# Kernel optimization log

Measured on AMD Instinct MI355X. Metric: run time of the kernel, lower is better.

## Reference

```python
import jax, jax.numpy as jnp
import numpy as np

ALPHA = 0.5  # distance-decay base (self.alpha)

def setup_inputs() -> dict:
    key = jax.random.key(0)
    N, E, D_IN, D_OUT = 50000, 800000, 128, 128
    k1, k2, k3, k4, k5 = jax.random.split(key, 5)
    h = jax.random.normal(k1, (N, D_IN), dtype=jnp.float32)
    # first N edges are self-loops so every node has in/out degree >= 1
    src = jnp.concatenate([jnp.arange(N), jax.random.randint(k2, (E - N,), 0, N)]).astype(jnp.int32)
    dst = jnp.concatenate([jnp.arange(N), jax.random.randint(k3, (E - N,), 0, N)]).astype(jnp.int32)
    distance = jax.random.randint(k4, (E,), 0, 6).astype(jnp.int32)
    limit = float(np.sqrt(6.0 / (D_IN + D_OUT)))  # xavier_uniform
    weight = jax.random.uniform(k5, (D_IN, D_OUT), jnp.float32, -limit, limit)
    bias = jnp.zeros((D_OUT,), jnp.float32)
    return {"h": h, "src": src, "dst": dst, "distance": distance, "weight": weight, "bias": bias}

def reference(h, src, dst, distance, weight, bias):
    N = h.shape[0]
    ones = jnp.ones(src.shape[0], jnp.float32)
    out_deg = jax.ops.segment_sum(ones, src, num_segments=N)  # [N]
    in_deg = jax.ops.segment_sum(ones, dst, num_segments=N)   # [N]
    # source-side symmetric norm
    feat = h * (out_deg ** -0.5)[:, None]                     # [N, D]
    # per-edge message: gathered src feature * alpha^distance
    w = jnp.power(jnp.float32(ALPHA), distance.astype(jnp.float32))  # [E]
    msg = feat[src] * w[:, None]                              # [E, D]
    # mean over mailbox == segment-sum / in-degree
    agg = jax.ops.segment_sum(msg, dst, num_segments=N) / in_deg[:, None]  # [N, D]
    rst = agg @ weight                                        # [N, D_OUT]
    rst = rst * (in_deg ** -0.5)[:, None] + bias
    return rst
```

## Files before the change

### kernel.cpp

```cpp
#include <hip/hip_runtime.h>


constexpr int D = 128;
constexpr int HC = 32;
constexpr int PNODES = 32;
constexpr int PCAP = 768;
constexpr int CHUNK = 8192;
constexpr int NCAST = 384;

typedef __attribute__((ext_vector_type(8))) short bf16x8;
typedef __attribute__((ext_vector_type(4))) float f32x4;
typedef __attribute__((ext_vector_type(2))) _Float16 f16x2;

__device__ __forceinline__ float bf16_to_f(unsigned int u16) {
    union { unsigned int u; float f; } c; c.u = u16 << 16; return c.f;
}
__device__ __forceinline__ unsigned int f_to_bf16(float f) {
    union { float f; unsigned int u; } c; c.f = f;
    unsigned int u = c.u;
    u += 0x7fffu + ((u >> 16) & 1u);
    return u >> 16;
}
__device__ __forceinline__ unsigned int pack_f16x2(float x, float y) {
    f16x2 p; p.x = (_Float16)x; p.y = (_Float16)y;
    union { f16x2 h; unsigned int u; } c; c.h = p; return c.u;
}

__global__ __launch_bounds__(256) void k_combo(const int* __restrict__ src,
        const int* __restrict__ dst, const int* __restrict__ dist,
        int* __restrict__ gcur, unsigned int* __restrict__ gbuf,
        unsigned int* __restrict__ gdeg,
        const float4* __restrict__ h4, uint4* __restrict__ hs4,
        const float* __restrict__ W, unsigned short* __restrict__ Wt,
        int E, int N, int NW, int hchunk, int P, int nbA) {
    extern __shared__ int dyn[];
    int tid = threadIdx.x;
    int bi = blockIdx.x;

    if (bi >= nbA + HC) {
        if (bi == nbA + HC) {
            for (int i = tid; i < D * D; i += 256) {
                int k = i >> 7, n = i & 127;
                Wt[n * D + k] = (unsigned short)f_to_bf16(W[i]);
            }
            return;
        }
        int cb = bi - (nbA + HC + 1);
        int G = N * (D / 8);
        for (int i = cb * 256 + tid; i < G; i += NCAST * 256) {
            float4 a = h4[2 * i];
            float4 b = h4[2 * i + 1];
            uint4 o;
            o.x = pack_f16x2(a.x, a.y);
            o.y = pack_f16x2(a.z, a.w);
            o.z = pack_f16x2(b.x, b.y);
            o.w = pack_f16x2(b.z, b.w);
            hs4[i] = o;
        }
        return;
    }

    if (bi >= nbA) {
        unsigned int* bins = (unsigned int*)dyn;
        for (int i = tid; i < NW; i += 256) bins[i] = 0;
        __syncthreads();
        int c = bi - nbA;
        int e0 = c * hchunk, e1 = min(e0 + hchunk, E);
        for (int i = e0 + tid * 4; i < e1; i += 1024) {
            if (i + 3 < e1) {
                int4 k4 = *(const int4*)&src[i];
                atomicAdd(&bins[k4.x >> 1], 1u << ((k4.x & 1) * 16));
                atomicAdd(&bins[k4.y >> 1], 1u << ((k4.y & 1) * 16));
                atomicAdd(&bins[k4.z >> 1], 1u << ((k4.z & 1) * 16));
                atomicAdd(&bins[k4.w >> 1], 1u << ((k4.w & 1) * 16));
            } else {
                for (int e = i; e < e1; e++)
                    atomicAdd(&bins[src[e] >> 1], 1u << ((src[e] & 1) * 16));
            }
        }
        __syncthreads();
        for (int i = tid; i < NW; i += 256) {
            unsigned int v = bins[i];
            if (v) atomicAdd(&gdeg[i], v);
        }
        return;
    }

    unsigned int* sorted = (unsigned int*)dyn;
    int* gidx  = dyn + CHUNK;
    int* hist  = dyn + 2 * CHUNK;
    int* start = hist + P;
    int* lofs  = start + P;
    int* base_g = lofs + P;
    __shared__ int wsum[4];

    int lane = tid & 63, w = tid >> 6;
    int e0 = bi * CHUNK;
    int e1 = min(e0 + CHUNK, E);
    int ce = e1 - e0;

    for (int b = tid; b < P; b += 256) hist[b] = 0;
    __syncthreads();

    for (int i = e0 + tid * 4; i < e1; i += 1024) {
        if (i + 3 < e1) {
            int4 d4 = *(const int4*)&dst[i];
            atomicAdd(&hist[d4.x >> 5], 1);
            atomicAdd(&hist[d4.y >> 5], 1);
            atomicAdd(&hist[d4.z >> 5], 1);
            atomicAdd(&hist[d4.w >> 5], 1);
        } else {
            for (int e = i; e < e1; e++) atomicAdd(&hist[dst[e] >> 5], 1);
        }
    }
    __syncthreads();

    int loc[7];
    int s = 0;
    #pragma unroll
    for (int j = 0; j < 7; j++) {
        int b = tid * 7 + j;
        int v = (b < P) ? hist[b] : 0;
        loc[j] = s;
        s += v;
    }
    int x = s;
    #pragma unroll
    for (int off = 1; off < 64; off <<= 1) {
        int t = __shfl_up(x, off, 64);
        if (lane >= off) x += t;
    }
    if (lane == 63) wsum[w] = x;
    __syncthreads();
    int tbase = x - s;
    #pragma unroll
    for (int k = 0; k < 4; k++) if (k < w) tbase += wsum[k];
    #pragma unroll
    for (int j = 0; j < 7; j++) {
        int b = tid * 7 + j;
        if (b < P) {
            int st = tbase + loc[j];
            start[b] = st;
            lofs[b] = st;
            int cnt = hist[b];
            if (cnt) base_g[b] = atomicAdd(&gcur[b], cnt);
        }
    }
    __syncthreads();

    for (int i = e0 + tid * 4; i < e1; i += 1024) {
        if (i + 3 < e1) {
            int4 s4 = *(const int4*)&src[i];
            int4 d4 = *(const int4*)&dst[i];
            int4 q4 = *(const int4*)&dist[i];
            #pragma unroll
            for (int j = 0; j < 4; j++) {
                int sv = (&s4.x)[j], dv = (&d4.x)[j], qv = (&q4.x)[j];
                int p = dv >> 5;
                unsigned int wd = (unsigned)sv | ((unsigned)(dv & 31) << 16)
                                | ((unsigned)qv << 21);
                int pos = atomicAdd(&lofs[p], 1);
                sorted[pos] = wd;
                int rank = base_g[p] + (pos - start[p]);
                gidx[pos] = (rank < PCAP) ? p * PCAP + rank : -1;
            }
        } else {
            for (int e = i; e < e1; e++) {
                int sv = src[e], dv = dst[e], qv = dist[e];
                int p = dv >> 5;
                unsigned int wd = (unsigned)sv | ((unsigned)(dv & 31) << 16)
                                | ((unsigned)qv << 21);
                int pos = atomicAdd(&lofs[p], 1);
                sorted[pos] = wd;
                int rank = base_g[p] + (pos - start[p]);
                gidx[pos] = (rank < PCAP) ? p * PCAP + rank : -1;
            }
        }
    }
    __syncthreads();

    for (int i = tid; i < ce; i += 256) {
        int g = gidx[i];
        if (g >= 0) gbuf[g] = sorted[i];
    }
}

__global__ __launch_bounds__(256, 6) void k_pagg(const uint4* __restrict__ hs4,
        const unsigned int* __restrict__ gbuf, const int* __restrict__ gcur,
        const unsigned short* __restrict__ gdeg16,
        const unsigned short* __restrict__ Wt, const float* __restrict__ bias,
        float* __restrict__ out, int N) {
    __shared__ unsigned int elist[PCAP];
    __shared__ unsigned int slist[PCAP];
    __shared__ float scoef[PCAP];
    __shared__ int h2[PNODES], st2[PNODES], lo2[PNODES];
    __shared__ unsigned short As[PNODES * 136];
    int p = blockIdx.x;
    int tid = threadIdx.x;
    int cnt = min(gcur[p], PCAP);
    const unsigned int* gp = gbuf + (size_t)p * PCAP;

    if (tid < PNODES) h2[tid] = 0;
    __syncthreads();
    for (int i = tid; i < cnt; i += 256) {
        unsigned int wd = gp[i];
        elist[i] = wd;
        atomicAdd(&h2[(wd >> 16) & 31], 1);
    }
    __syncthreads();
    if (tid < 64) {
        int v = (tid < PNODES) ? h2[tid] : 0;
        int x = v;
        #pragma unroll
        for (int off = 1; off < 32; off <<= 1) {
            int t = __shfl_up(x, off, 64);
            if ((tid & 63) >= off) x += t;
        }
        if (tid < PNODES) { st2[tid] = x - v; lo2[tid] = x - v; }
    }
    __syncthreads();
    for (int i = tid; i < cnt; i += 256) {
        unsigned int wd = elist[i];
        int pos = atomicAdd(&lo2[(wd >> 16) & 31], 1);
        slist[pos] = wd;
        unsigned int sv = wd & 0xffffu;
        float os = rsqrtf((float)gdeg16[sv]);
        scoef[pos] = __uint_as_float((127u - ((wd >> 21) & 7u)) << 23) * os;
    }
    __syncthreads();

    int wv = tid >> 6, l64 = tid & 63;
    int lane16 = l64 & 15, sub = l64 >> 4;
    #pragma unroll
    for (int k = 0; k < 8; k++) {
        int dl = wv * 8 + k;
        int node = p * PNODES + dl;
        int deg = h2[dl], b = st2[dl];
        float acc[8] = {0.f, 0.f, 0.f, 0.f, 0.f, 0.f, 0.f, 0.f};
        for (int eo = 0; eo < deg; eo += 32) {
            uint4 hv[8];
            float cc[8];
            #pragma unroll
            for (int j = 0; j < 8; j++) {
                if (eo + j * 4 < deg) {
                    int off = eo + j * 4 + sub;
                    bool valid = off < deg;
                    int ei = b + (valid ? off : 0);
                    unsigned int wd = slist[ei];
                    float c0 = scoef[ei];
                    cc[j] = valid ? c0 : 0.f;
                    hv[j] = hs4[((wd & 0xffffu) << 4) + (unsigned)lane16];
                }
            }
            #pragma unroll
            for (int j = 0; j < 8; j++) {
                if (eo + j * 4 < deg) {
                    float c = cc[j];
                    const f16x2* hp = (const f16x2*)&hv[j];
                    #pragma unroll
                    for (int q = 0; q < 4; q++) {
                        acc[2 * q]     = fmaf((float)hp[q].x, c, acc[2 * q]);
                        acc[2 * q + 1] = fmaf((float)hp[q].y, c, acc[2 * q + 1]);
                    }
                }
            }
        }
        #pragma unroll
        for (int j = 0; j < 8; j++) {
            acc[j] += __shfl_xor(acc[j], 16, 64);
            acc[j] += __shfl_xor(acc[j], 32, 64);
        }
        if (sub == 0) {
            uint4 o = make_uint4(0u, 0u, 0u, 0u);
            if (node < N) {
                float fd = (float)deg;
                float sc = rsqrtf(fd) / fd;
                o.x = f_to_bf16(acc[0] * sc) | (f_to_bf16(acc[1] * sc) << 16);
                o.y = f_to_bf16(acc[2] * sc) | (f_to_bf16(acc[3] * sc) << 16);
                o.z = f_to_bf16(acc[4] * sc) | (f_to_bf16(acc[5] * sc) << 16);
                o.w = f_to_bf16(acc[6] * sc) | (f_to_bf16(acc[7] * sc) << 16);
            }
            *(uint4*)&As[dl * 136 + lane16 * 8] = o;
        }
    }
    __syncthreads();

    int m = l64 & 15, quad = l64 >> 4;
    int mt = wv & 1, ntb = (wv >> 1) * 4;
    f32x4 acc2[4];
    #pragma unroll
    for (int t = 0; t < 4; t++) acc2[t] = (f32x4){0.f, 0.f, 0.f, 0.f};
    #pragma unroll
    for (int s = 0; s < 4; s++) {
        bf16x8 a = *(const bf16x8*)&As[(mt * 16 + m) * 136 + quad * 8 + s * 32];
        #pragma unroll
        for (int t = 0; t < 4; t++) {
            int n = (ntb + t) * 16 + m;
            bf16x8 b = *(const bf16x8*)&Wt[n * D + quad * 8 + s * 32];
            acc2[t] = __builtin_amdgcn_mfma_f32_16x16x32_bf16(a, b, acc2[t], 0, 0, 0);
        }
    }
    int orow0 = p * PNODES + mt * 16 + quad * 4;
    #pragma unroll
    for (int t = 0; t < 4; t++) {
        int n = (ntb + t) * 16 + m;
        float bz = bias[n];
        #pragma unroll
        for (int r = 0; r < 4; r++) {
            int grow = orow0 + r;
            if (grow < N) out[(size_t)grow * D + n] = acc2[t][r] + bz;
        }
    }
}

extern "C" void kernel_launch(void* const* d_in, const int* in_sizes, int n_in,
                              void* d_out, int out_size, void* d_ws, size_t ws_size,
                              hipStream_t stream) {
    const float* h    = (const float*)d_in[0];
    const int*   src  = (const int*)d_in[1];
    const int*   dst  = (const int*)d_in[2];
    const int*   dist = (const int*)d_in[3];
    const float* W    = (const float*)d_in[4];
    const float* bias = (const float*)d_in[5];
    float* out = (float*)d_out;
    const int N = in_sizes[0] / D;
    const int E = in_sizes[1];

    const int NW = (N + 1) / 2;
    const int hchunk = (((E + HC - 1) / HC) + 3) & ~3;
    const int P = (N + PNODES - 1) / PNODES;
    const int nbA = (E + CHUNK - 1) / CHUNK;

    char* ws = (char*)d_ws;
    size_t p = 0;
    auto alloc = [&](size_t bytes) -> char* {
        char* r = ws + p;
        p = (p + bytes + 511) & ~(size_t)511;
        return r;
    };
    int* gcur = (int*)alloc((size_t)P * 4);
    unsigned int* gdeg = (unsigned int*)alloc((size_t)NW * 4);
    unsigned int* gbuf = (unsigned int*)alloc((size_t)P * PCAP * 4);
    unsigned short* hs = (unsigned short*)alloc((size_t)N * D * 2);
    unsigned short* Wt = (unsigned short*)alloc((size_t)D * D * 2);

    size_t dyn_part = ((size_t)2 * CHUNK + 4 * P) * 4;
    size_t dyn_hist = (size_t)NW * 4;
    size_t dyn_sz = dyn_part > dyn_hist ? dyn_part : dyn_hist;

    hipMemsetAsync(gcur, 0, (size_t)((char*)gdeg - (char*)gcur) + (size_t)NW * 4,
                   stream);
    k_combo<<<nbA + HC + 1 + NCAST, 256, dyn_sz, stream>>>(src, dst, dist,
            gcur, gbuf, gdeg, (const float4*)h, (uint4*)hs, W, Wt,
            E, N, NW, hchunk, P, nbA);
    k_pagg<<<P, 256, 0, stream>>>((const uint4*)hs, gbuf, gcur,
            (const unsigned short*)gdeg, Wt, bias, out, N);
}
```

Baseline: 155.5 us.

## Double-buffer neighbor feature gathers through LDS with async global_load_lds

The per-node gather loop in the aggregation kernel is replaced with a software pipeline. It issues asynchronous global-to-LDS loads for the next 16-edge batch, possibly belonging to the next node, while the current batch is accumulated from LDS. It flattens the per-node loop across node boundaries and skips zero-degree nodes, whose rows are zeroed separately. This costs 32KB of extra shared memory per block and lowers the launch-bounds occupancy hint from 6 to 3, trading occupancy-based latency hiding for explicit prefetch.

```diff
diff --git a/kernel.cpp b/kernel.cpp
--- a/kernel.cpp
+++ b/kernel.cpp
@@ -24,6 +24,11 @@
 __device__ __forceinline__ unsigned int pack_f16x2(float x, float y) {
     f16x2 p; p.x = (_Float16)x; p.y = (_Float16)y;
     union { f16x2 h; unsigned int u; } c; c.h = p; return c.u;
+}
+__device__ __forceinline__ void gload16(const void* g, void* l) {
+    __builtin_amdgcn_global_load_lds(
+        (const __attribute__((address_space(1))) void*)g,
+        (__attribute__((address_space(3))) void*)l, 16, 0, 0);
 }
 
 __global__ __launch_bounds__(256) void k_combo(const int* __restrict__ src,
@@ -185,7 +190,7 @@
     }
 }
 
-__global__ __launch_bounds__(256, 6) void k_pagg(const uint4* __restrict__ hs4,
+__global__ __launch_bounds__(256, 3) void k_pagg(const uint4* __restrict__ hs4,
         const unsigned int* __restrict__ gbuf, const int* __restrict__ gcur,
         const unsigned short* __restrict__ gdeg16,
         const unsigned short* __restrict__ Wt, const float* __restrict__ bias,
@@ -195,6 +200,7 @@
     __shared__ float scoef[PCAP];
     __shared__ int h2[PNODES], st2[PNODES], lo2[PNODES];
     __shared__ unsigned short As[PNODES * 136];
+    __shared__ char stage[4 * 2 * 4096];
     int p = blockIdx.x;
     int tid = threadIdx.x;
     int cnt = min(gcur[p], PCAP);
@@ -231,57 +237,77 @@
 
     int wv = tid >> 6, l64 = tid & 63;
     int lane16 = l64 & 15, sub = l64 >> 4;
-    #pragma unroll
-    for (int k = 0; k < 8; k++) {
-        int dl = wv * 8 + k;
-        int node = p * PNODES + dl;
-        int deg = h2[dl], b = st2[dl];
-        float acc[8] = {0.f, 0.f, 0.f, 0.f, 0.f, 0.f, 0.f, 0.f};
-        for (int eo = 0; eo < deg; eo += 32) {
-            uint4 hv[8];
-            float cc[8];
+    int wb = wv * 8;
+    char* swave = stage + wv * 8192;
+
+    auto issue = [&](char* lbase, int b, int deg, int eo) {
+        #pragma unroll
+        for (int i = 0; i < 4; i++) {
+            int s = eo + i * 4 + sub;
+            int ei = b + min(s, deg - 1);
+            unsigned int sv = slist[ei] & 0xffffu;
+            gload16(&hs4[(sv << 4) + (unsigned)lane16], lbase + i * 1024);
+        }
+    };
+
+    int k = 0;
+    while (k < 8 && h2[wb + k] == 0) k++;
+    int eo = 0, buf = 0;
+    if (k < 8) issue(swave, st2[wb + k], h2[wb + k], 0);
+    float acc[8] = {0.f, 0.f, 0.f, 0.f, 0.f, 0.f, 0.f, 0.f};
+    while (k < 8) {
+        int deg = h2[wb + k], b = st2[wb + k];
+        int kn = k, eon = eo + 16;
+        if (eon >= deg) {
+            eon = 0; kn = k + 1;
+            while (kn < 8 && h2[wb + kn] == 0) kn++;
+        }
+        bool hn = kn < 8;
+        if (hn) issue(swave + (buf ^ 1) * 4096, st2[wb + kn], h2[wb + kn], eon);
+        if (hn) asm volatile("s_waitcnt vmcnt(4)" ::: "memory");
+        else    asm volatile("s_waitcnt vmcnt(0)" ::: "memory");
+        const char* cbase = swave + buf * 4096;
+        #pragma unroll
+        for (int j = 0; j < 4; j++) {
+            int s = eo + j * 4 + sub;
+            bool valid = s < deg;
+            uint4 hv = *(const uint4*)(cbase + (j * 4 + sub) * 256 + lane16 * 16);
+            float c = scoef[b + min(s, deg - 1)];
+            c = valid ? c : 0.f;
+            const f16x2* hp = (const f16x2*)&hv;
+            #pragma unroll
+            for (int q = 0; q < 4; q++) {
+                acc[2 * q]     = fmaf((float)hp[q].x, c, acc[2 * q]);
+                acc[2 * q + 1] = fmaf((float)hp[q].y, c, acc[2 * q + 1]);
+            }
+        }
+        if (eo + 16 >= deg) {
             #pragma unroll
             for (int j = 0; j < 8; j++) {
-                if (eo + j * 4 < deg) {
-                    int off = eo + j * 4 + sub;
-                    bool valid = off < deg;
-                    int ei = b + (valid ? off : 0);
-                    unsigned int wd = slist[ei];
-                    float c0 = scoef[ei];
-                    cc[j] = valid ? c0 : 0.f;
-                    hv[j] = hs4[((wd & 0xffffu) << 4) + (unsigned)lane16];
+                acc[j] += __shfl_xor(acc[j], 16, 64);
+                acc[j] += __shfl_xor(acc[j], 32, 64);
+            }
+            if (sub == 0) {
+                uint4 o = make_uint4(0u, 0u, 0u, 0u);
+                if (p * PNODES + wb + k < N) {
+                    float fd = (float)deg;
+                    float sc = rsqrtf(fd) / fd;
+                    o.x = f_to_bf16(acc[0] * sc) | (f_to_bf16(acc[1] * sc) << 16);
+                    o.y = f_to_bf16(acc[2] * sc) | (f_to_bf16(acc[3] * sc) << 16);
+                    o.z = f_to_bf16(acc[4] * sc) | (f_to_bf16(acc[5] * sc) << 16);
+                    o.w = f_to_bf16(acc[6] * sc) | (f_to_bf16(acc[7] * sc) << 16);
                 }
+                *(uint4*)&As[(wb + k) * 136 + lane16 * 8] = o;
             }
             #pragma unroll
-            for (int j = 0; j < 8; j++) {
-                if (eo + j * 4 < deg) {
-                    float c = cc[j];
-                    const f16x2* hp = (const f16x2*)&hv[j];
-                    #pragma unroll
-                    for (int q = 0; q < 4; q++) {
-                        acc[2 * q]     = fmaf((float)hp[q].x, c, acc[2 * q]);
-                        acc[2 * q + 1] = fmaf((float)hp[q].y, c, acc[2 * q + 1]);
-                    }
-                }
-            }
-        }
-        #pragma unroll
-        for (int j = 0; j < 8; j++) {
-            acc[j] += __shfl_xor(acc[j], 16, 64);
-            acc[j] += __shfl_xor(acc[j], 32, 64);
-        }
-        if (sub == 0) {
-            uint4 o = make_uint4(0u, 0u, 0u, 0u);
-            if (node < N) {
-                float fd = (float)deg;
-                float sc = rsqrtf(fd) / fd;
-                o.x = f_to_bf16(acc[0] * sc) | (f_to_bf16(acc[1] * sc) << 16);
-                o.y = f_to_bf16(acc[2] * sc) | (f_to_bf16(acc[3] * sc) << 16);
-                o.z = f_to_bf16(acc[4] * sc) | (f_to_bf16(acc[5] * sc) << 16);
-                o.w = f_to_bf16(acc[6] * sc) | (f_to_bf16(acc[7] * sc) << 16);
-            }
-            *(uint4*)&As[dl * 136 + lane16 * 8] = o;
-        }
+            for (int j = 0; j < 8; j++) acc[j] = 0.f;
+        }
+        k = kn; eo = eon; buf ^= 1;
+    }
+    #pragma unroll
+    for (int kk = 0; kk < 8; kk++) {
+        if (h2[wb + kk] == 0 && sub == 0)
+            *(uint4*)&As[(wb + kk) * 136 + lane16 * 8] = make_uint4(0u, 0u, 0u, 0u);
     }
     __syncthreads();
 
```

New measurement: 183.8 us. +18.2%, slower.

## Split degree histogram into node halves to shrink LDS and raise occupancy

Applied to the files above, without the earlier changes.

The out-degree histogram blocks are split into two groups, each covering half of the node-word range. This halves the dynamic LDS each histogram block needs, so the shared-memory footprint of the fused kernel drops, and more blocks should fit per CU. The edge chunk size is reduced to keep the partition LDS in line, and the aggregation kernel's launch bounds now request higher occupancy. In exchange every edge's src is read twice, there are twice as many histogram blocks, and the tighter register budget may cause spills.

```diff
diff --git a/kernel.cpp b/kernel.cpp
--- a/kernel.cpp
+++ b/kernel.cpp
@@ -5,7 +5,7 @@
 constexpr int HC = 32;
 constexpr int PNODES = 32;
 constexpr int PCAP = 768;
-constexpr int CHUNK = 8192;
+constexpr int CHUNK = 6144;
 constexpr int NCAST = 384;
 
 typedef __attribute__((ext_vector_type(8))) short bf16x8;
@@ -32,20 +32,20 @@
         unsigned int* __restrict__ gdeg,
         const float4* __restrict__ h4, uint4* __restrict__ hs4,
         const float* __restrict__ W, unsigned short* __restrict__ Wt,
-        int E, int N, int NW, int hchunk, int P, int nbA) {
+        int E, int N, int NW, int NWH, int hchunk, int P, int nbA) {
     extern __shared__ int dyn[];
     int tid = threadIdx.x;
     int bi = blockIdx.x;
 
-    if (bi >= nbA + HC) {
-        if (bi == nbA + HC) {
+    if (bi >= nbA + 2 * HC) {
+        if (bi == nbA + 2 * HC) {
             for (int i = tid; i < D * D; i += 256) {
                 int k = i >> 7, n = i & 127;
                 Wt[n * D + k] = (unsigned short)f_to_bf16(W[i]);
             }
             return;
         }
-        int cb = bi - (nbA + HC + 1);
+        int cb = bi - (nbA + 2 * HC + 1);
         int G = N * (D / 8);
         for (int i = cb * 256 + tid; i < G; i += NCAST * 256) {
             float4 a = h4[2 * i];
@@ -62,26 +62,37 @@
 
     if (bi >= nbA) {
         unsigned int* bins = (unsigned int*)dyn;
-        for (int i = tid; i < NW; i += 256) bins[i] = 0;
+        int c = bi - nbA;
+        int half = c >> 5;
+        int cc = c & 31;
+        int wlo = half * NWH;
+        int whi = min(wlo + NWH, NW);
+        int nwh = whi - wlo;
+        for (int i = tid; i < nwh; i += 256) bins[i] = 0;
         __syncthreads();
-        int c = bi - nbA;
-        int e0 = c * hchunk, e1 = min(e0 + hchunk, E);
+        int e0 = cc * hchunk, e1 = min(e0 + hchunk, E);
         for (int i = e0 + tid * 4; i < e1; i += 1024) {
             if (i + 3 < e1) {
                 int4 k4 = *(const int4*)&src[i];
-                atomicAdd(&bins[k4.x >> 1], 1u << ((k4.x & 1) * 16));
-                atomicAdd(&bins[k4.y >> 1], 1u << ((k4.y & 1) * 16));
-                atomicAdd(&bins[k4.z >> 1], 1u << ((k4.z & 1) * 16));
-                atomicAdd(&bins[k4.w >> 1], 1u << ((k4.w & 1) * 16));
+                #pragma unroll
+                for (int j = 0; j < 4; j++) {
+                    int sv = (&k4.x)[j];
+                    int wi = sv >> 1;
+                    if (wi >= wlo && wi < whi)
+                        atomicAdd(&bins[wi - wlo], 1u << ((sv & 1) * 16));
+                }
             } else {
-                for (int e = i; e < e1; e++)
-                    atomicAdd(&bins[src[e] >> 1], 1u << ((src[e] & 1) * 16));
+                for (int e = i; e < e1; e++) {
+                    int wi = src[e] >> 1;
+                    if (wi >= wlo && wi < whi)
+                        atomicAdd(&bins[wi - wlo], 1u << ((src[e] & 1) * 16));
+                }
             }
         }
         __syncthreads();
-        for (int i = tid; i < NW; i += 256) {
+        for (int i = tid; i < nwh; i += 256) {
             unsigned int v = bins[i];
-            if (v) atomicAdd(&gdeg[i], v);
+            if (v) atomicAdd(&gdeg[wlo + i], v);
         }
         return;
     }
@@ -185,7 +196,7 @@
     }
 }
 
-__global__ __launch_bounds__(256, 6) void k_pagg(const uint4* __restrict__ hs4,
+__global__ __launch_bounds__(256, 8) void k_pagg(const uint4* __restrict__ hs4,
         const unsigned int* __restrict__ gbuf, const int* __restrict__ gcur,
         const unsigned short* __restrict__ gdeg16,
         const unsigned short* __restrict__ Wt, const float* __restrict__ bias,
@@ -327,6 +338,7 @@
     const int E = in_sizes[1];
 
     const int NW = (N + 1) / 2;
+    const int NWH = (NW + 1) / 2;
     const int hchunk = (((E + HC - 1) / HC) + 3) & ~3;
     const int P = (N + PNODES - 1) / PNODES;
     const int nbA = (E + CHUNK - 1) / CHUNK;
@@ -345,14 +357,14 @@
     unsigned short* Wt = (unsigned short*)alloc((size_t)D * D * 2);
 
     size_t dyn_part = ((size_t)2 * CHUNK + 4 * P) * 4;
-    size_t dyn_hist = (size_t)NW * 4;
+    size_t dyn_hist = (size_t)NWH * 4;
     size_t dyn_sz = dyn_part > dyn_hist ? dyn_part : dyn_hist;
 
     hipMemsetAsync(gcur, 0, (size_t)((char*)gdeg - (char*)gcur) + (size_t)NW * 4,
                    stream);
-    k_combo<<<nbA + HC + 1 + NCAST, 256, dyn_sz, stream>>>(src, dst, dist,
+    k_combo<<<nbA + 2 * HC + 1 + NCAST, 256, dyn_sz, stream>>>(src, dst, dist,
             gcur, gbuf, gdeg, (const float4*)h, (uint4*)hs, W, Wt,
-            E, N, NW, hchunk, P, nbA);
+            E, N, NW, NWH, hchunk, P, nbA);
     k_pagg<<<P, 256, 0, stream>>>((const uint4*)hs, gbuf, gcur,
             (const unsigned short*)gdeg, Wt, bias, out, N);
 }
```

Result: no change. 153.2 us (-1.4%).
